# Kernel optimization log

Hardware: AMD Instinct MI355X
Metric: run time of the kernel (lower is better)

The kernel has to match this reference:

```python
import jax, jax.numpy as jnp
import numpy as np

N = 500000   # nodes (total bases across sequences)
E = 2 * N    # edges, degree-2 sequence graph
F = 128      # filters
BN_EPS = 1e-3  # Keras BatchNormalization default epsilon


def setup_inputs() -> dict:
    key = jax.random.key(0)
    ks = jax.random.split(key, 10)
    x = jax.random.normal(ks[0], (N, F), jnp.float32)
    # segment ids: sorted, each node appears twice (tf.math.segment_sum requires sorted ids)
    seg = jnp.repeat(jnp.arange(N, dtype=jnp.int32), 2)
    pairs_prev = jnp.stack([seg, jax.random.randint(ks[1], (E,), 0, N, jnp.int32)], axis=1)
    pairs_next = jnp.stack([seg, jax.random.randint(ks[2], (E,), 0, N, jnp.int32)], axis=1)
    s = 0.05  # 'random_normal' initializer stddev
    wNext = jax.random.normal(ks[3], (F, F), jnp.float32) * s
    wPrev = jax.random.normal(ks[4], (F, F), jnp.float32) * s
    b = jnp.zeros((1, F), jnp.float32)
    # GRUCell(F): kernel [F,3F], recurrent_kernel [F,3F], bias [2,3F] (reset_after=True)
    gru_kernel = jax.random.normal(ks[5], (F, 3 * F), jnp.float32) * s
    gru_recurrent_kernel = jax.random.normal(ks[6], (F, 3 * F), jnp.float32) * s
    gru_bias = jnp.zeros((2, 3 * F), jnp.float32)
    bn_gamma = jnp.ones((F,), jnp.float32)
    bn_beta = jnp.zeros((F,), jnp.float32)
    bn_mean = jax.random.normal(ks[7], (F,), jnp.float32) * 0.05
    bn_var = jnp.ones((F,), jnp.float32) + jax.random.uniform(ks[8], (F,), jnp.float32) * 0.1
    return {"x": x, "pairs_prev": pairs_prev, "pairs_next": pairs_next,
            "wNext": wNext, "wPrev": wPrev, "b": b,
            "gru_kernel": gru_kernel, "gru_recurrent_kernel": gru_recurrent_kernel,
            "gru_bias": gru_bias, "bn_gamma": bn_gamma, "bn_beta": bn_beta,
            "bn_mean": bn_mean, "bn_var": bn_var}


def reference(x, pairs_prev, pairs_next, wNext, wPrev, b,
              gru_kernel, gru_recurrent_kernel, gru_bias,
              bn_gamma, bn_beta, bn_mean, bn_var):
    n = x.shape[0]
    # gather neighbor features + segment_sum aggregation
    prev_sumx = jax.ops.segment_sum(x[pairs_prev[:, 1]], pairs_prev[:, 0], num_segments=n)
    next_sumx = jax.ops.segment_sum(x[pairs_next[:, 1]], pairs_next[:, 0], num_segments=n)
    # aggre = next@Wn + prev@Wp + b ; non-padded, multiply=False -> + x
    aggre = next_sumx @ wNext + prev_sumx @ wPrev + b + x
    # activation then BatchNorm (inference mode, training=False)
    a = jax.nn.relu(aggre)
    a = bn_gamma * (a - bn_mean) * jax.lax.rsqrt(bn_var + BN_EPS) + bn_beta
    # GRUCell(F) update with state h = x (Keras reset_after=True)
    mx = a @ gru_kernel + gru_bias[0]        # [N, 3F]
    mh = x @ gru_recurrent_kernel + gru_bias[1]
    xz, xr, xh = jnp.split(mx, 3, axis=-1)
    rz, rr, rh = jnp.split(mh, 3, axis=-1)
    z = jax.nn.sigmoid(xz + rz)
    r = jax.nn.sigmoid(xr + rr)
    hh = jnp.tanh(xh + r * rh)
    return z * x + (1.0 - z) * hh
```

## Files before the change

### kernel.cpp

```cpp
#include <hip/hip_runtime.h>
#include <hip/hip_bf16.h>
#include <stdint.h>

#define FDIM 128
#define AS1 __attribute__((address_space(1)))
#define AS3 __attribute__((address_space(3)))

typedef short bf16x8 __attribute__((ext_vector_type(8)));
typedef float f32x4 __attribute__((ext_vector_type(4)));
typedef float f32x2 __attribute__((ext_vector_type(2)));

__device__ __forceinline__ unsigned short f2bf(float f) {
    union { float f; unsigned int u; } v; v.f = f;
    unsigned int r = v.u + 0x7FFFu + ((v.u >> 16) & 1u);
    return (unsigned short)(r >> 16);
}
__device__ __forceinline__ unsigned int pack2bf(float a, float b) {
    return (unsigned int)f2bf(a) | ((unsigned int)f2bf(b) << 16);
}
__device__ __forceinline__ float bf2f(unsigned short u) {
    union { unsigned int u; float f; } v; v.u = (unsigned int)u << 16; return v.f;
}
__device__ __forceinline__ uint2 sum4fp8(unsigned int w0, unsigned int w1) {
    f32x2 a0 = __builtin_amdgcn_cvt_pk_f32_fp8((int)w0, false);
    f32x2 a1 = __builtin_amdgcn_cvt_pk_f32_fp8((int)w0, true);
    f32x2 b0 = __builtin_amdgcn_cvt_pk_f32_fp8((int)w1, false);
    f32x2 b1 = __builtin_amdgcn_cvt_pk_f32_fp8((int)w1, true);
    float s0 = a0.x + b0.x, s1 = a0.y + b0.y;
    float s2 = a1.x + b1.x, s3 = a1.y + b1.y;
    uint2 r;
    asm("v_cvt_pk_bf16_f32 %0, %1, %2" : "=v"(r.x) : "v"(s0), "v"(s1));
    asm("v_cvt_pk_bf16_f32 %0, %1, %2" : "=v"(r.y) : "v"(s2), "v"(s3));
    return r;
}

__global__ void prep_kernel(const float* __restrict__ wNext, const float* __restrict__ wPrev,
                            const float* __restrict__ gk, const float* __restrict__ gr,
                            const float* __restrict__ gb, const float* __restrict__ gamma,
                            const float* __restrict__ beta, const float* __restrict__ mean,
                            const float* __restrict__ var,
                            unsigned short* __restrict__ bt1, unsigned short* __restrict__ bt2,
                            float* __restrict__ bias2, float* __restrict__ bnscale,
                            float* __restrict__ bnshift)
{
    int t = blockIdx.x * blockDim.x + threadIdx.x;
    if (t < 32768) {
        int n = t >> 8, k = t & 255;
        float v = (k < 128) ? wNext[k * 128 + n] : wPrev[(k - 128) * 128 + n];
        unsigned int byte = (unsigned)n * 512u + (((unsigned)(k * 2)) ^ (((unsigned)(n & 15)) << 4));
        *(unsigned short*)((unsigned char*)bt1 + byte) = f2bf(v);
    } else if (t < 32768 + 131072) {
        int e = t - 32768;
        int n = e >> 8, k = e & 255;
        float v;
        if (n < 256)      v = (k < 128) ? gk[k * 384 + n] : gr[(k - 128) * 384 + n];
        else if (n < 384) v = (k < 128) ? gk[k * 384 + n] : 0.f;
        else              v = (k < 128) ? 0.f : gr[(k - 128) * 384 + (n - 128)];
        int g = n >> 7, fl = n & 127;
        int nn = ((fl >> 4) << 6) + (g << 4) + (fl & 15);
        unsigned int byte = (unsigned)nn * 512u + (((unsigned)(k * 2)) ^ (((unsigned)(nn & 15)) << 4));
        *(unsigned short*)((unsigned char*)bt2 + byte) = f2bf(v);
    } else if (t < 32768 + 131072 + 512) {
        int n = t - (32768 + 131072);
        float v;
        if (n < 256)      v = gb[n] + gb[384 + n];
        else if (n < 384) v = gb[n];
        else              v = gb[384 + (n - 128)];
        bias2[n] = v;
    } else if (t < 32768 + 131072 + 512 + 128) {
        int f = t - (32768 + 131072 + 512);
        float s = gamma[f] * rsqrtf(var[f] + 1e-3f);
        bnscale[f] = s;
        bnshift[f] = beta[f] - mean[f] * s;
    }
}

__global__ __launch_bounds__(256) void x_convert(const float* __restrict__ x,
                                                 unsigned short* __restrict__ xbf,
                                                 unsigned char* __restrict__ xq, int Nn)
{
    const int total = Nn * 16;
    const float4* x4 = (const float4*)x;
    for (int t = blockIdx.x * 256 + threadIdx.x; t < total; t += gridDim.x * 256) {
        int m = t >> 4, l = t & 15;
        float4 v0 = x4[m * 32 + l * 2];
        float4 v1 = x4[m * 32 + l * 2 + 1];
        uint4 pk;
        pk.x = pack2bf(v0.x, v0.y); pk.y = pack2bf(v0.z, v0.w);
        pk.z = pack2bf(v1.x, v1.y); pk.w = pack2bf(v1.z, v1.w);
        unsigned int byte = (unsigned)m * 256u + (((unsigned)(l * 16)) ^ (((unsigned)(m & 15)) << 4));
        *(uint4*)((unsigned char*)xbf + byte) = pk;
        int q0 = __builtin_amdgcn_cvt_pk_fp8_f32(v0.x, v0.y, 0, false);
        q0 = __builtin_amdgcn_cvt_pk_fp8_f32(v0.z, v0.w, q0, true);
        int q1 = __builtin_amdgcn_cvt_pk_fp8_f32(v1.x, v1.y, 0, false);
        q1 = __builtin_amdgcn_cvt_pk_fp8_f32(v1.z, v1.w, q1, true);
        uint2 qq; qq.x = (unsigned)q0; qq.y = (unsigned)q1;
        *(uint2*)(xq + (size_t)m * 128u + (unsigned)(l * 8)) = qq;
    }
}

__attribute__((amdgpu_waves_per_eu(4, 8)))
__global__ __launch_bounds__(512) void k_gather_g1(
    const unsigned short* __restrict__ xbf, const unsigned char* __restrict__ xq,
    const int* __restrict__ pprev, const int* __restrict__ pnext,
    const unsigned short* __restrict__ bt1,
    const float* __restrict__ bvec, const float* __restrict__ bnscale,
    const float* __restrict__ bnshift,
    unsigned short* __restrict__ a_out, int Nn)
{
    __shared__ __align__(16) unsigned char lds[49152];
    const int tid = threadIdx.x, wid = tid >> 6, lane = tid & 63;
    const int col0 = lane & 15, kq = lane >> 4;
    const unsigned int rs = (unsigned)col0 << 4;

    const unsigned char* bt1b = (const unsigned char*)bt1;
    bf16x8 b1[8];
#pragma unroll
    for (int kk = 0; kk < 8; kk++)
        b1[kk] = *(const bf16x8*)(bt1b + (unsigned)(wid * 16 + col0) * 512u +
                                  (((unsigned)(kk * 64 + kq * 16)) ^ rs));
#pragma unroll
    for (int kk = 0; kk < 8; kk++) asm volatile("" : "+v"(b1[kk]));

    const int f = wid * 16 + col0;
    const float bb = bvec[f], sc = bnscale[f], sh = bnshift[f];

    const int rg = tid >> 3, s8 = tid & 7, dirp = s8 >> 2, pg = s8 & 3;
    const int* pid = dirp ? pprev : pnext;
    const unsigned char* xb = (const unsigned char*)xbf;

    const int G = (int)gridDim.x;
    const int tiles = (Nn + 63) >> 6;

    uint4 q0a, q0b, q1a, q1b;
    int4 idxA = {0, 0, 0, 0}, idxB;
    { int gn = blockIdx.x * 64 + rg; if (gn < Nn) idxA = *(const int4*)(pid + (size_t)4 * gn); }

    for (int t = blockIdx.x; t < tiles; t += G) {
        const int base = t * 64;
        {
            size_t xg = (size_t)base * 256u + (unsigned)(wid * 2048) + (unsigned)(lane * 16);
            __builtin_amdgcn_global_load_lds((const AS1 unsigned int*)(xb + xg),
                (AS3 unsigned int*)(lds + 32768u + (unsigned)(wid * 2048)), 16, 0, 0);
            __builtin_amdgcn_global_load_lds((const AS1 unsigned int*)(xb + xg + 1024),
                (AS3 unsigned int*)(lds + 32768u + (unsigned)(wid * 2048) + 1024u), 16, 0, 0);
        }
        {
            const unsigned char* r0 = xq + (size_t)idxA.y * 128u + (unsigned)(pg * 32);
            const unsigned char* r1 = xq + (size_t)idxA.w * 128u + (unsigned)(pg * 32);
            q0a = *(const uint4*)(r0);
            q0b = *(const uint4*)(r0 + 16);
            q1a = *(const uint4*)(r1);
            q1b = *(const uint4*)(r1 + 16);
        }
        __builtin_amdgcn_sched_barrier(0);
        idxB = (int4){0, 0, 0, 0};
        {
            int gn = (t + G) * 64 + rg;
            if (t + G < tiles && gn < Nn) idxB = *(const int4*)(pid + (size_t)4 * gn);
        }
        __builtin_amdgcn_sched_barrier(0);
        asm volatile("s_waitcnt vmcnt(1)" ::: "memory");
        __builtin_amdgcn_sched_barrier(0);
        {
            unsigned char* Sd = lds + (unsigned)(rg * 512 + dirp * 256);
            unsigned swd = ((unsigned)(rg & 15)) << 4;
            uint2 e0, e1;
            uint4 d;
            e0 = sum4fp8(q0a.x, q1a.x); e1 = sum4fp8(q0a.y, q1a.y);
            d.x = e0.x; d.y = e0.y; d.z = e1.x; d.w = e1.y;
            *(uint4*)(Sd + (((unsigned)(pg * 64 + 0)) ^ swd)) = d;
            e0 = sum4fp8(q0a.z, q1a.z); e1 = sum4fp8(q0a.w, q1a.w);
            d.x = e0.x; d.y = e0.y; d.z = e1.x; d.w = e1.y;
            *(uint4*)(Sd + (((unsigned)(pg * 64 + 16)) ^ swd)) = d;
            e0 = sum4fp8(q0b.x, q1b.x); e1 = sum4fp8(q0b.y, q1b.y);
            d.x = e0.x; d.y = e0.y; d.z = e1.x; d.w = e1.y;
            *(uint4*)(Sd + (((unsigned)(pg * 64 + 32)) ^ swd)) = d;
            e0 = sum4fp8(q0b.z, q1b.z); e1 = sum4fp8(q0b.w, q1b.w);
            d.x = e0.x; d.y = e0.y; d.z = e1.x; d.w = e1.y;
            *(uint4*)(Sd + (((unsigned)(pg * 64 + 48)) ^ swd)) = d;
        }
        asm volatile("s_waitcnt lgkmcnt(0)" ::: "memory");
        __builtin_amdgcn_sched_barrier(0);
        __builtin_amdgcn_s_barrier();

        f32x4 acc1[4];
#pragma unroll
        for (int m = 0; m < 4; m++) acc1[m] = (f32x4){bb, bb, bb, bb};
#pragma unroll
        for (int kk = 0; kk < 8; kk++) {
            unsigned ko = ((unsigned)(kk * 64 + kq * 16)) ^ rs;
            bf16x8 a0 = *(const bf16x8*)(lds + (unsigned)(0 * 16 + col0) * 512u + ko);
            bf16x8 a1 = *(const bf16x8*)(lds + (unsigned)(1 * 16 + col0) * 512u + ko);
            bf16x8 a2 = *(const bf16x8*)(lds + (unsigned)(2 * 16 + col0) * 512u + ko);
            bf16x8 a3 = *(const bf16x8*)(lds + (unsigned)(3 * 16 + col0) * 512u + ko);
            acc1[0] = __builtin_amdgcn_mfma_f32_16x16x32_bf16(a0, b1[kk], acc1[0], 0, 0, 0);
            acc1[1] = __builtin_amdgcn_mfma_f32_16x16x32_bf16(a1, b1[kk], acc1[1], 0, 0, 0);
            acc1[2] = __builtin_amdgcn_mfma_f32_16x16x32_bf16(a2, b1[kk], acc1[2], 0, 0, 0);
            acc1[3] = __builtin_amdgcn_mfma_f32_16x16x32_bf16(a3, b1[kk], acc1[3], 0, 0, 0);
        }
        {
            const unsigned char* X = lds + 32768u;
#pragma unroll
            for (int m = 0; m < 4; m++) {
#pragma unroll
                for (int i = 0; i < 4; i++) {
                    int r = m * 16 + kq * 4 + i;
                    int grow = base + r;
                    if (grow < Nn) {
                        unsigned sw = ((unsigned)(r & 15)) << 4;
                        unsigned co = ((unsigned)(f * 2)) ^ sw;
                        float xv = bf2f(*(const unsigned short*)(X + (unsigned)r * 256u + co));
                        float v = acc1[m][i] + xv;
                        v = fmaxf(v, 0.f) * sc + sh;
                        __builtin_nontemporal_store(
                            f2bf(v),
                            (unsigned short*)((unsigned char*)a_out + (size_t)grow * 256u + co));
                    }
                }
            }
        }
        __builtin_amdgcn_s_barrier();
        idxA = idxB;
    }
}

__attribute__((amdgpu_waves_per_eu(2, 2)))
__global__ __launch_bounds__(512) void k_g2_gru(
    const unsigned short* __restrict__ a_in, const unsigned short* __restrict__ xbf,
    const unsigned short* __restrict__ bt2p, const float* __restrict__ bias2,
    float* __restrict__ out, int Nn)
{
    __shared__ __align__(16) unsigned char lds[65536];
    const int tid = threadIdx.x, wid = tid >> 6, lane = tid & 63;
    const int col0 = lane & 15, kq = lane >> 4;
    const unsigned int rs = (unsigned)col0 << 4;

    const unsigned char* bt2b = (const unsigned char*)bt2p;
    bf16x8 b2z[8], b2r[8], b2xh[4], b2rh[4];
#pragma unroll
    for (int kk = 0; kk < 8; kk++) {
        b2z[kk] = *(const bf16x8*)(bt2b + (unsigned)(wid * 64 + 0 + col0) * 512u + (((unsigned)(kk * 64 + kq * 16)) ^ rs));
        b2r[kk] = *(const bf16x8*)(bt2b + (unsigned)(wid * 64 + 16 + col0) * 512u + (((unsigned)(kk * 64 + kq * 16)) ^ rs));
    }
#pragma unroll
    for (int kk = 0; kk < 4; kk++) {
        b2xh[kk] = *(const bf16x8*)(bt2b + (unsigned)(wid * 64 + 32 + col0) * 512u + (((unsigned)(kk * 64 + kq * 16)) ^ rs));
        b2rh[kk] = *(const bf16x8*)(bt2b + (unsigned)(wid * 64 + 48 + col0) * 512u + (((unsigned)((kk + 4) * 64 + kq * 16)) ^ rs));
    }
#pragma unroll
    for (int kk = 0; kk < 8; kk++) {
        asm volatile("" : "+v"(b2z[kk]));
        asm volatile("" : "+v"(b2r[kk]));
    }
#pragma unroll
    for (int kk = 0; kk < 4; kk++) {
        asm volatile("" : "+v"(b2xh[kk]));
        asm volatile("" : "+v"(b2rh[kk]));
    }

    const int f = wid * 16 + col0;
    const float cz = bias2[f], cr = bias2[128 + f], cxh = bias2[256 + f], crh = bias2[384 + f];

    const unsigned char* aB = (const unsigned char*)a_in;
    const unsigned char* xB = (const unsigned char*)xbf;
    const int G = (int)gridDim.x;
    const int tiles = (Nn + 63) >> 6;

#define STAGE2(tt, pp) do {                                                                  \
    size_t g_ = (size_t)(tt) * 16384u + (unsigned)(wid * 2048) + (unsigned)(lane * 16);      \
    unsigned o_ = (unsigned)(pp) * 32768u + (unsigned)(wid * 2048);                          \
    __builtin_amdgcn_global_load_lds((const AS1 unsigned int*)(aB + g_),                     \
                                     (AS3 unsigned int*)(lds + o_), 16, 0, 0);               \
    __builtin_amdgcn_global_load_lds((const AS1 unsigned int*)(aB + g_ + 1024),              \
                                     (AS3 unsigned int*)(lds + o_ + 1024), 16, 0, 0);        \
    __builtin_amdgcn_global_load_lds((const AS1 unsigned int*)(xB + g_),                     \
                                     (AS3 unsigned int*)(lds + o_ + 16384u), 16, 0, 0);      \
    __builtin_amdgcn_global_load_lds((const AS1 unsigned int*)(xB + g_ + 1024),              \
                                     (AS3 unsigned int*)(lds + o_ + 16384u + 1024), 16, 0, 0);\
} while (0)

    STAGE2(blockIdx.x, 0);
    asm volatile("s_waitcnt vmcnt(0)" ::: "memory");
    __builtin_amdgcn_sched_barrier(0);
    __builtin_amdgcn_s_barrier();

    int p = 0;
    for (int t = blockIdx.x; t < tiles; t += G) {
        const int base = t * 64;
        {
            int tn = t + G;
            int tc = (tn < tiles) ? tn : t;
            STAGE2(tc, p ^ 1);
        }
        const unsigned char* A_ = lds + (unsigned)p * 32768u;
        const unsigned char* X_ = lds + (unsigned)p * 32768u + 16384u;

#pragma unroll
        for (int half = 0; half < 2; half++) {
            f32x4 az[2], ar[2], axh[2], arh[2];
#pragma unroll
            for (int mm = 0; mm < 2; mm++) {
                az[mm]  = (f32x4){cz, cz, cz, cz};
                ar[mm]  = (f32x4){cr, cr, cr, cr};
                axh[mm] = (f32x4){cxh, cxh, cxh, cxh};
                arh[mm] = (f32x4){crh, crh, crh, crh};
            }
#pragma unroll
            for (int kk = 0; kk < 8; kk++) {
                bf16x8 a2f[2];
#pragma unroll
                for (int mm = 0; mm < 2; mm++) {
                    int m = half * 2 + mm;
                    if (kk < 4)
                        a2f[mm] = *(const bf16x8*)(A_ + (unsigned)(m * 16 + col0) * 256u +
                                                   (((unsigned)(kk * 64 + kq * 16)) ^ rs));
                    else
                        a2f[mm] = *(const bf16x8*)(X_ + (unsigned)(m * 16 + col0) * 256u +
                                                   (((unsigned)((kk - 4) * 64 + kq * 16)) ^ rs));
                }
#pragma unroll
                for (int mm = 0; mm < 2; mm++) {
                    az[mm] = __builtin_amdgcn_mfma_f32_16x16x32_bf16(a2f[mm], b2z[kk], az[mm], 0, 0, 0);
                    ar[mm] = __builtin_amdgcn_mfma_f32_16x16x32_bf16(a2f[mm], b2r[kk], ar[mm], 0, 0, 0);
                    if (kk < 4)
                        axh[mm] = __builtin_amdgcn_mfma_f32_16x16x32_bf16(a2f[mm], b2xh[kk], axh[mm], 0, 0, 0);
                    else
                        arh[mm] = __builtin_amdgcn_mfma_f32_16x16x32_bf16(a2f[mm], b2rh[kk - 4], arh[mm], 0, 0, 0);
                }
            }
#pragma unroll
            for (int mm = 0; mm < 2; mm++) {
                int m = half * 2 + mm;
#pragma unroll
                for (int i = 0; i < 4; i++) {
                    int r = m * 16 + kq * 4 + i;
                    int grow = base + r;
                    if (grow < Nn) {
                        float z  = __builtin_amdgcn_rcpf(1.f + __expf(-az[mm][i]));
                        float rr = __builtin_amdgcn_rcpf(1.f + __expf(-ar[mm][i]));
                        float u  = axh[mm][i] + rr * arh[mm][i];
                        float th = 1.f - 2.f * __builtin_amdgcn_rcpf(__expf(2.f * u) + 1.f);
                        unsigned sw = ((unsigned)(r & 15)) << 4;
                        float xv = bf2f(*(const unsigned short*)(X_ + (unsigned)r * 256u +
                                                                 (((unsigned)(f * 2)) ^ sw)));
                        __builtin_nontemporal_store(th + z * (xv - th),
                                                    out + (size_t)grow * FDIM + f);
                    }
                }
            }
        }
        asm volatile("s_waitcnt vmcnt(16) lgkmcnt(0)" ::: "memory");
        __builtin_amdgcn_sched_barrier(0);
        __builtin_amdgcn_s_barrier();
        p ^= 1;
    }
#undef STAGE2
}

extern "C" void kernel_launch(void* const* d_in, const int* in_sizes, int n_in,
                              void* d_out, int out_size, void* d_ws, size_t ws_size,
                              hipStream_t stream)
{
    const float* x      = (const float*)d_in[0];
    const int*   pprev  = (const int*)d_in[1];
    const int*   pnext  = (const int*)d_in[2];
    const float* wNext  = (const float*)d_in[3];
    const float* wPrev  = (const float*)d_in[4];
    const float* b      = (const float*)d_in[5];
    const float* gk     = (const float*)d_in[6];
    const float* gr     = (const float*)d_in[7];
    const float* gb     = (const float*)d_in[8];
    const float* gamma  = (const float*)d_in[9];
    const float* beta   = (const float*)d_in[10];
    const float* mean   = (const float*)d_in[11];
    const float* var    = (const float*)d_in[12];
    float* out = (float*)d_out;
    const int Nn = in_sizes[0] / FDIM;

    unsigned char* ws = (unsigned char*)d_ws;
    unsigned short* xbf  = (unsigned short*)(ws + 0);
    unsigned short* a_ws = (unsigned short*)(ws + (size_t)Nn * 256u);
    unsigned char*  xq   = (unsigned char*)(ws + (size_t)Nn * 512u);
    size_t off_bt = (size_t)Nn * 640u;
    unsigned short* bt1   = (unsigned short*)(ws + off_bt);
    unsigned short* bt2   = (unsigned short*)(ws + off_bt + 65536);
    float* bias2          = (float*)(ws + off_bt + 327680);
    float* bnscale        = (float*)(ws + off_bt + 327680 + 2048);
    float* bnshift        = (float*)(ws + off_bt + 327680 + 2048 + 512);

    prep_kernel<<<643, 256, 0, stream>>>(wNext, wPrev, gk, gr, gb, gamma, beta, mean, var,
                                         bt1, bt2, bias2, bnscale, bnshift);
    x_convert<<<2048, 256, 0, stream>>>(x, xbf, xq, Nn);
    k_gather_g1<<<768, 512, 0, stream>>>(xbf, xq, pprev, pnext, bt1, b, bnscale, bnshift, a_ws, Nn);
    k_g2_gru<<<256, 512, 0, stream>>>(a_ws, xbf, bt2, bias2, out, Nn);
}
```

Measured before the change: 330.1 us.

## Software-pipeline neighbor gather and x staging one tile ahead in gather kernel

Restructures the gather+GEMM1 loop so the fp8 neighbor gathers and index loads for the next tile (and indices two tiles ahead) are issued before the current tile's MFMA work. x tiles are double-buffered in LDS, which grows from 48KB to 64KB, so the async x copy for tile t+G overlaps the current tile's compute and epilogue. The goal is to hide random-gather latency behind compute. The larger LDS footprint reduces occupancy, and the grid shrinks from 768 to 512 blocks to match. Hand-tuned vmcnt waits must match the exact load counts, which is fragile.

```diff
diff --git a/kernel.cpp b/kernel.cpp
--- a/kernel.cpp
+++ b/kernel.cpp
@@ -108,7 +108,7 @@
     const float* __restrict__ bnshift,
     unsigned short* __restrict__ a_out, int Nn)
 {
-    __shared__ __align__(16) unsigned char lds[49152];
+    __shared__ __align__(16) unsigned char lds[65536];
     const int tid = threadIdx.x, wid = tid >> 6, lane = tid & 63;
     const int col0 = lane & 15, kq = lane >> 4;
     const unsigned int rs = (unsigned)col0 << 4;
@@ -133,56 +133,77 @@
     const int tiles = (Nn + 63) >> 6;
 
     uint4 q0a, q0b, q1a, q1b;
-    int4 idxA = {0, 0, 0, 0}, idxB;
-    { int gn = blockIdx.x * 64 + rg; if (gn < Nn) idxA = *(const int4*)(pid + (size_t)4 * gn); }
-
+    int4 idxN, idxN2;
+
+#define STAGE_X(tt, slot) do {                                                              \
+    size_t xg_ = (size_t)(tt) * 16384u + (unsigned)(wid * 2048) + (unsigned)(lane * 16);    \
+    unsigned xo_ = 32768u + (unsigned)(slot) * 16384u + (unsigned)(wid * 2048);             \
+    __builtin_amdgcn_global_load_lds((const AS1 unsigned int*)(xb + xg_),                   \
+                                     (AS3 unsigned int*)(lds + xo_), 16, 0, 0);             \
+    __builtin_amdgcn_global_load_lds((const AS1 unsigned int*)(xb + xg_ + 1024),            \
+                                     (AS3 unsigned int*)(lds + xo_ + 1024), 16, 0, 0);      \
+} while (0)
+
+#define GATHER_ISSUE(ix) do {                                                               \
+    const unsigned char* r0_ = xq + (size_t)(ix).y * 128u + (unsigned)(pg * 32);            \
+    const unsigned char* r1_ = xq + (size_t)(ix).w * 128u + (unsigned)(pg * 32);            \
+    q0a = *(const uint4*)(r0_);                                                             \
+    q0b = *(const uint4*)(r0_ + 16);                                                        \
+    q1a = *(const uint4*)(r1_);                                                             \
+    q1b = *(const uint4*)(r1_ + 16);                                                        \
+} while (0)
+
+#define IDX_LOAD(dst, tc) do {                                                              \
+    (dst) = (int4){0, 0, 0, 0};                                                             \
+    int gn_ = (tc) * 64 + rg;                                                               \
+    if ((tc) < tiles && gn_ < Nn) (dst) = *(const int4*)(pid + (size_t)4 * gn_);            \
+} while (0)
+
+#define SUM_WRITE() do {                                                                    \
+    unsigned char* Sd_ = lds + (unsigned)(rg * 512 + dirp * 256);                           \
+    unsigned swd_ = ((unsigned)(rg & 15)) << 4;                                             \
+    uint2 e0_, e1_; uint4 d_;                                                               \
+    e0_ = sum4fp8(q0a.x, q1a.x); e1_ = sum4fp8(q0a.y, q1a.y);                               \
+    d_.x = e0_.x; d_.y = e0_.y; d_.z = e1_.x; d_.w = e1_.y;                                 \
+    *(uint4*)(Sd_ + (((unsigned)(pg * 64 + 0)) ^ swd_)) = d_;                               \
+    e0_ = sum4fp8(q0a.z, q1a.z); e1_ = sum4fp8(q0a.w, q1a.w);                               \
+    d_.x = e0_.x; d_.y = e0_.y; d_.z = e1_.x; d_.w = e1_.y;                                 \
+    *(uint4*)(Sd_ + (((unsigned)(pg * 64 + 16)) ^ swd_)) = d_;                              \
+    e0_ = sum4fp8(q0b.x, q1b.x); e1_ = sum4fp8(q0b.y, q1b.y);                               \
+    d_.x = e0_.x; d_.y = e0_.y; d_.z = e1_.x; d_.w = e1_.y;                                 \
+    *(uint4*)(Sd_ + (((unsigned)(pg * 64 + 32)) ^ swd_)) = d_;                              \
+    e0_ = sum4fp8(q0b.z, q1b.z); e1_ = sum4fp8(q0b.w, q1b.w);                               \
+    d_.x = e0_.x; d_.y = e0_.y; d_.z = e1_.x; d_.w = e1_.y;                                 \
+    *(uint4*)(Sd_ + (((unsigned)(pg * 64 + 48)) ^ swd_)) = d_;                              \
+} while (0)
+
+    {
+        int4 idx0 = (int4){0, 0, 0, 0};
+        int gn = blockIdx.x * 64 + rg;
+        if (gn < Nn) idx0 = *(const int4*)(pid + (size_t)4 * gn);
+        GATHER_ISSUE(idx0);
+        IDX_LOAD(idxN, (int)blockIdx.x + G);
+        STAGE_X(blockIdx.x, 0);
+        __builtin_amdgcn_sched_barrier(0);
+        asm volatile("s_waitcnt vmcnt(0)" ::: "memory");
+        __builtin_amdgcn_sched_barrier(0);
+        SUM_WRITE();
+        asm volatile("s_waitcnt lgkmcnt(0)" ::: "memory");
+        __builtin_amdgcn_sched_barrier(0);
+        __builtin_amdgcn_s_barrier();
+    }
+
+    int xs = 0;
     for (int t = blockIdx.x; t < tiles; t += G) {
         const int base = t * 64;
+        GATHER_ISSUE(idxN);
+        IDX_LOAD(idxN2, t + 2 * G);
+        __builtin_amdgcn_sched_barrier(0);
         {
-            size_t xg = (size_t)base * 256u + (unsigned)(wid * 2048) + (unsigned)(lane * 16);
-            __builtin_amdgcn_global_load_lds((const AS1 unsigned int*)(xb + xg),
-                (AS3 unsigned int*)(lds + 32768u + (unsigned)(wid * 2048)), 16, 0, 0);
-            __builtin_amdgcn_global_load_lds((const AS1 unsigned int*)(xb + xg + 1024),
-                (AS3 unsigned int*)(lds + 32768u + (unsigned)(wid * 2048) + 1024u), 16, 0, 0);
+            int tc = t + G; if (tc >= tiles) tc = t;
+            STAGE_X(tc, xs ^ 1);
         }
-        {
-            const unsigned char* r0 = xq + (size_t)idxA.y * 128u + (unsigned)(pg * 32);
-            const unsigned char* r1 = xq + (size_t)idxA.w * 128u + (unsigned)(pg * 32);
-            q0a = *(const uint4*)(r0);
-            q0b = *(const uint4*)(r0 + 16);
-            q1a = *(const uint4*)(r1);
-            q1b = *(const uint4*)(r1 + 16);
-        }
-        __builtin_amdgcn_sched_barrier(0);
-        idxB = (int4){0, 0, 0, 0};
-        {
-            int gn = (t + G) * 64 + rg;
-            if (t + G < tiles && gn < Nn) idxB = *(const int4*)(pid + (size_t)4 * gn);
-        }
-        __builtin_amdgcn_sched_barrier(0);
-        asm volatile("s_waitcnt vmcnt(1)" ::: "memory");
-        __builtin_amdgcn_sched_barrier(0);
-        {
-            unsigned char* Sd = lds + (unsigned)(rg * 512 + dirp * 256);
-            unsigned swd = ((unsigned)(rg & 15)) << 4;
-            uint2 e0, e1;
-            uint4 d;
-            e0 = sum4fp8(q0a.x, q1a.x); e1 = sum4fp8(q0a.y, q1a.y);
-            d.x = e0.x; d.y = e0.y; d.z = e1.x; d.w = e1.y;
-            *(uint4*)(Sd + (((unsigned)(pg * 64 + 0)) ^ swd)) = d;
-            e0 = sum4fp8(q0a.z, q1a.z); e1 = sum4fp8(q0a.w, q1a.w);
-            d.x = e0.x; d.y = e0.y; d.z = e1.x; d.w = e1.y;
-            *(uint4*)(Sd + (((unsigned)(pg * 64 + 16)) ^ swd)) = d;
-            e0 = sum4fp8(q0b.x, q1b.x); e1 = sum4fp8(q0b.y, q1b.y);
-            d.x = e0.x; d.y = e0.y; d.z = e1.x; d.w = e1.y;
-            *(uint4*)(Sd + (((unsigned)(pg * 64 + 32)) ^ swd)) = d;
-            e0 = sum4fp8(q0b.z, q1b.z); e1 = sum4fp8(q0b.w, q1b.w);
-            d.x = e0.x; d.y = e0.y; d.z = e1.x; d.w = e1.y;
-            *(uint4*)(Sd + (((unsigned)(pg * 64 + 48)) ^ swd)) = d;
-        }
-        asm volatile("s_waitcnt lgkmcnt(0)" ::: "memory");
-        __builtin_amdgcn_sched_barrier(0);
-        __builtin_amdgcn_s_barrier();
+        __builtin_amdgcn_sched_barrier(0);
 
         f32x4 acc1[4];
 #pragma unroll
@@ -200,7 +221,7 @@
             acc1[3] = __builtin_amdgcn_mfma_f32_16x16x32_bf16(a3, b1[kk], acc1[3], 0, 0, 0);
         }
         {
-            const unsigned char* X = lds + 32768u;
+            const unsigned char* X = lds + 32768u + (unsigned)xs * 16384u;
 #pragma unroll
             for (int m = 0; m < 4; m++) {
 #pragma unroll
@@ -220,9 +241,23 @@
                 }
             }
         }
+        __builtin_amdgcn_sched_barrier(0);
+        asm volatile("s_waitcnt vmcnt(18) lgkmcnt(0)" ::: "memory");
+        __builtin_amdgcn_sched_barrier(0);
         __builtin_amdgcn_s_barrier();
-        idxA = idxB;
-    }
+        SUM_WRITE();
+        asm volatile("s_waitcnt lgkmcnt(0)" ::: "memory");
+        __builtin_amdgcn_sched_barrier(0);
+        asm volatile("s_waitcnt vmcnt(16)" ::: "memory");
+        __builtin_amdgcn_sched_barrier(0);
+        __builtin_amdgcn_s_barrier();
+        xs ^= 1;
+        idxN = idxN2;
+    }
+#undef STAGE_X
+#undef GATHER_ISSUE
+#undef IDX_LOAD
+#undef SUM_WRITE
 }
 
 __attribute__((amdgpu_waves_per_eu(2, 2)))
@@ -392,6 +427,6 @@
     prep_kernel<<<643, 256, 0, stream>>>(wNext, wPrev, gk, gr, gb, gamma, beta, mean, var,
                                          bt1, bt2, bias2, bnscale, bnshift);
     x_convert<<<2048, 256, 0, stream>>>(x, xbf, xq, Nn);
-    k_gather_g1<<<768, 512, 0, stream>>>(xbf, xq, pprev, pnext, bt1, b, bnscale, bnshift, a_ws, Nn);
+    k_gather_g1<<<512, 512, 0, stream>>>(xbf, xq, pprev, pnext, bt1, b, bnscale, bnshift, a_ws, Nn);
     k_g2_gru<<<256, 512, 0, stream>>>(a_ws, xbf, bt2, bias2, out, Nn);
 }
```

Measured after the change: 407.4 us. 1.23x slower.

## Warp-specialize gather kernel into producer and MFMA consumer waves with double-buffered LDS

Applied to the files above, without the earlier changes.

The fused gather+GEMM kernel is split so that waves 0-3 only gather the fp8 neighbour rows, sum them into LDS and copy the x tile, while waves 4-7 only run the bf16 MFMA and the ReLU/BN epilogue. Each consumer wave now covers 32 output columns. The tile shrinks from 64 to 32 rows and the LDS staging is double-buffered, so the gather for tile k+1 can overlap the matrix multiply for tile k with one barrier per tile. The grid drops from 768 to 512 blocks. The risks are that only half the waves issue gather loads, and the smaller tile raises barrier and per-tile overhead.

```diff
diff --git a/kernel.cpp b/kernel.cpp
--- a/kernel.cpp
+++ b/kernel.cpp
@@ -110,118 +110,147 @@
 {
     __shared__ __align__(16) unsigned char lds[49152];
     const int tid = threadIdx.x, wid = tid >> 6, lane = tid & 63;
-    const int col0 = lane & 15, kq = lane >> 4;
-    const unsigned int rs = (unsigned)col0 << 4;
-
-    const unsigned char* bt1b = (const unsigned char*)bt1;
-    bf16x8 b1[8];
-#pragma unroll
-    for (int kk = 0; kk < 8; kk++)
-        b1[kk] = *(const bf16x8*)(bt1b + (unsigned)(wid * 16 + col0) * 512u +
-                                  (((unsigned)(kk * 64 + kq * 16)) ^ rs));
-#pragma unroll
-    for (int kk = 0; kk < 8; kk++) asm volatile("" : "+v"(b1[kk]));
-
-    const int f = wid * 16 + col0;
-    const float bb = bvec[f], sc = bnscale[f], sh = bnshift[f];
-
-    const int rg = tid >> 3, s8 = tid & 7, dirp = s8 >> 2, pg = s8 & 3;
-    const int* pid = dirp ? pprev : pnext;
-    const unsigned char* xb = (const unsigned char*)xbf;
-
     const int G = (int)gridDim.x;
-    const int tiles = (Nn + 63) >> 6;
-
-    uint4 q0a, q0b, q1a, q1b;
-    int4 idxA = {0, 0, 0, 0}, idxB;
-    { int gn = blockIdx.x * 64 + rg; if (gn < Nn) idxA = *(const int4*)(pid + (size_t)4 * gn); }
-
-    for (int t = blockIdx.x; t < tiles; t += G) {
-        const int base = t * 64;
-        {
-            size_t xg = (size_t)base * 256u + (unsigned)(wid * 2048) + (unsigned)(lane * 16);
-            __builtin_amdgcn_global_load_lds((const AS1 unsigned int*)(xb + xg),
-                (AS3 unsigned int*)(lds + 32768u + (unsigned)(wid * 2048)), 16, 0, 0);
-            __builtin_amdgcn_global_load_lds((const AS1 unsigned int*)(xb + xg + 1024),
-                (AS3 unsigned int*)(lds + 32768u + (unsigned)(wid * 2048) + 1024u), 16, 0, 0);
-        }
-        {
-            const unsigned char* r0 = xq + (size_t)idxA.y * 128u + (unsigned)(pg * 32);
-            const unsigned char* r1 = xq + (size_t)idxA.w * 128u + (unsigned)(pg * 32);
-            q0a = *(const uint4*)(r0);
-            q0b = *(const uint4*)(r0 + 16);
-            q1a = *(const uint4*)(r1);
-            q1b = *(const uint4*)(r1 + 16);
-        }
-        __builtin_amdgcn_sched_barrier(0);
-        idxB = (int4){0, 0, 0, 0};
-        {
-            int gn = (t + G) * 64 + rg;
-            if (t + G < tiles && gn < Nn) idxB = *(const int4*)(pid + (size_t)4 * gn);
-        }
-        __builtin_amdgcn_sched_barrier(0);
-        asm volatile("s_waitcnt vmcnt(1)" ::: "memory");
-        __builtin_amdgcn_sched_barrier(0);
-        {
-            unsigned char* Sd = lds + (unsigned)(rg * 512 + dirp * 256);
-            unsigned swd = ((unsigned)(rg & 15)) << 4;
-            uint2 e0, e1;
-            uint4 d;
-            e0 = sum4fp8(q0a.x, q1a.x); e1 = sum4fp8(q0a.y, q1a.y);
-            d.x = e0.x; d.y = e0.y; d.z = e1.x; d.w = e1.y;
-            *(uint4*)(Sd + (((unsigned)(pg * 64 + 0)) ^ swd)) = d;
-            e0 = sum4fp8(q0a.z, q1a.z); e1 = sum4fp8(q0a.w, q1a.w);
-            d.x = e0.x; d.y = e0.y; d.z = e1.x; d.w = e1.y;
-            *(uint4*)(Sd + (((unsigned)(pg * 64 + 16)) ^ swd)) = d;
-            e0 = sum4fp8(q0b.x, q1b.x); e1 = sum4fp8(q0b.y, q1b.y);
-            d.x = e0.x; d.y = e0.y; d.z = e1.x; d.w = e1.y;
-            *(uint4*)(Sd + (((unsigned)(pg * 64 + 32)) ^ swd)) = d;
-            e0 = sum4fp8(q0b.z, q1b.z); e1 = sum4fp8(q0b.w, q1b.w);
-            d.x = e0.x; d.y = e0.y; d.z = e1.x; d.w = e1.y;
-            *(uint4*)(Sd + (((unsigned)(pg * 64 + 48)) ^ swd)) = d;
-        }
-        asm volatile("s_waitcnt lgkmcnt(0)" ::: "memory");
-        __builtin_amdgcn_sched_barrier(0);
+    const int tiles = (Nn + 31) >> 5;
+    const int bid = (int)blockIdx.x;
+    const int ntb = (tiles - bid + G - 1) / G;
+
+    if (wid < 4) {
+        const int ptid = tid;
+        const int rg = ptid >> 3, s8 = ptid & 7, dirp = s8 >> 2, pg = s8 & 3;
+        const int* pid = dirp ? pprev : pnext;
+        const unsigned char* xb = (const unsigned char*)xbf;
+
+        uint4 q0a, q0b, q1a, q1b;
+        int4 idxA = {0, 0, 0, 0}, idxB;
+        { int gn = bid * 32 + rg; if (gn < Nn) idxA = *(const int4*)(pid + (size_t)4 * gn); }
+
+        for (int k = 0; k < ntb; k++) {
+            const int t = bid + k * G;
+            const int dstp = k & 1;
+            {
+                size_t xg = (size_t)t * 8192u + (unsigned)(ptid * 16);
+                unsigned xo = 32768u + (unsigned)dstp * 8192u + (unsigned)(ptid * 16);
+                __builtin_amdgcn_global_load_lds((const AS1 unsigned int*)(xb + xg),
+                                                 (AS3 unsigned int*)(lds + xo), 16, 0, 0);
+                __builtin_amdgcn_global_load_lds((const AS1 unsigned int*)(xb + xg + 4096),
+                                                 (AS3 unsigned int*)(lds + xo + 4096), 16, 0, 0);
+            }
+            {
+                const unsigned char* r0 = xq + (size_t)idxA.y * 128u + (unsigned)(pg * 32);
+                const unsigned char* r1 = xq + (size_t)idxA.w * 128u + (unsigned)(pg * 32);
+                q0a = *(const uint4*)(r0);
+                q0b = *(const uint4*)(r0 + 16);
+                q1a = *(const uint4*)(r1);
+                q1b = *(const uint4*)(r1 + 16);
+            }
+            __builtin_amdgcn_sched_barrier(0);
+            idxB = (int4){0, 0, 0, 0};
+            {
+                int tn = t + G;
+                int gn = tn * 32 + rg;
+                if (tn < tiles && gn < Nn) idxB = *(const int4*)(pid + (size_t)4 * gn);
+            }
+            __builtin_amdgcn_sched_barrier(0);
+            asm volatile("s_waitcnt vmcnt(1)" ::: "memory");
+            __builtin_amdgcn_sched_barrier(0);
+            {
+                unsigned char* Sd = lds + (unsigned)dstp * 16384u + (unsigned)(rg * 512 + dirp * 256);
+                unsigned swd = ((unsigned)(rg & 15)) << 4;
+                uint2 e0, e1;
+                uint4 d;
+                e0 = sum4fp8(q0a.x, q1a.x); e1 = sum4fp8(q0a.y, q1a.y);
+                d.x = e0.x; d.y = e0.y; d.z = e1.x; d.w = e1.y;
+                *(uint4*)(Sd + (((unsigned)(pg * 64 + 0)) ^ swd)) = d;
+                e0 = sum4fp8(q0a.z, q1a.z); e1 = sum4fp8(q0a.w, q1a.w);
+                d.x = e0.x; d.y = e0.y; d.z = e1.x; d.w = e1.y;
+                *(uint4*)(Sd + (((unsigned)(pg * 64 + 16)) ^ swd)) = d;
+                e0 = sum4fp8(q0b.x, q1b.x); e1 = sum4fp8(q0b.y, q1b.y);
+                d.x = e0.x; d.y = e0.y; d.z = e1.x; d.w = e1.y;
+                *(uint4*)(Sd + (((unsigned)(pg * 64 + 32)) ^ swd)) = d;
+                e0 = sum4fp8(q0b.z, q1b.z); e1 = sum4fp8(q0b.w, q1b.w);
+                d.x = e0.x; d.y = e0.y; d.z = e1.x; d.w = e1.y;
+                *(uint4*)(Sd + (((unsigned)(pg * 64 + 48)) ^ swd)) = d;
+            }
+            asm volatile("s_waitcnt lgkmcnt(0)" ::: "memory");
+            __builtin_amdgcn_sched_barrier(0);
+            idxA = idxB;
+            __builtin_amdgcn_s_barrier();
+        }
         __builtin_amdgcn_s_barrier();
-
-        f32x4 acc1[4];
-#pragma unroll
-        for (int m = 0; m < 4; m++) acc1[m] = (f32x4){bb, bb, bb, bb};
+    } else {
+        const int cw = wid - 4;
+        const int col0 = lane & 15, kq = lane >> 4;
+        const unsigned int rs = (unsigned)col0 << 4;
+        const unsigned char* bt1b = (const unsigned char*)bt1;
+
+        bf16x8 b1a[8], b1b[8];
 #pragma unroll
         for (int kk = 0; kk < 8; kk++) {
-            unsigned ko = ((unsigned)(kk * 64 + kq * 16)) ^ rs;
-            bf16x8 a0 = *(const bf16x8*)(lds + (unsigned)(0 * 16 + col0) * 512u + ko);
-            bf16x8 a1 = *(const bf16x8*)(lds + (unsigned)(1 * 16 + col0) * 512u + ko);
-            bf16x8 a2 = *(const bf16x8*)(lds + (unsigned)(2 * 16 + col0) * 512u + ko);
-            bf16x8 a3 = *(const bf16x8*)(lds + (unsigned)(3 * 16 + col0) * 512u + ko);
-            acc1[0] = __builtin_amdgcn_mfma_f32_16x16x32_bf16(a0, b1[kk], acc1[0], 0, 0, 0);
-            acc1[1] = __builtin_amdgcn_mfma_f32_16x16x32_bf16(a1, b1[kk], acc1[1], 0, 0, 0);
-            acc1[2] = __builtin_amdgcn_mfma_f32_16x16x32_bf16(a2, b1[kk], acc1[2], 0, 0, 0);
-            acc1[3] = __builtin_amdgcn_mfma_f32_16x16x32_bf16(a3, b1[kk], acc1[3], 0, 0, 0);
-        }
-        {
-            const unsigned char* X = lds + 32768u;
-#pragma unroll
-            for (int m = 0; m < 4; m++) {
+            b1a[kk] = *(const bf16x8*)(bt1b + (unsigned)(cw * 32 + col0) * 512u +
+                                       (((unsigned)(kk * 64 + kq * 16)) ^ rs));
+            b1b[kk] = *(const bf16x8*)(bt1b + (unsigned)(cw * 32 + 16 + col0) * 512u +
+                                       (((unsigned)(kk * 64 + kq * 16)) ^ rs));
+        }
+#pragma unroll
+        for (int kk = 0; kk < 8; kk++) {
+            asm volatile("" : "+v"(b1a[kk]));
+            asm volatile("" : "+v"(b1b[kk]));
+        }
+
+        const int f0 = cw * 32 + col0, f1 = f0 + 16;
+        const float bb0 = bvec[f0], sc0 = bnscale[f0], sh0 = bnshift[f0];
+        const float bb1 = bvec[f1], sc1 = bnscale[f1], sh1 = bnshift[f1];
+
+        for (int k = 0; k < ntb; k++) {
+            __builtin_amdgcn_s_barrier();
+            const int t = bid + k * G;
+            const int p = k & 1;
+            const unsigned char* S = lds + (unsigned)p * 16384u;
+            const unsigned char* X = lds + 32768u + (unsigned)p * 8192u;
+
+            f32x4 acc00 = (f32x4){bb0, bb0, bb0, bb0};
+            f32x4 acc01 = (f32x4){bb1, bb1, bb1, bb1};
+            f32x4 acc10 = (f32x4){bb0, bb0, bb0, bb0};
+            f32x4 acc11 = (f32x4){bb1, bb1, bb1, bb1};
+#pragma unroll
+            for (int kk = 0; kk < 8; kk++) {
+                unsigned ko = ((unsigned)(kk * 64 + kq * 16)) ^ rs;
+                bf16x8 a0 = *(const bf16x8*)(S + (unsigned)(col0) * 512u + ko);
+                bf16x8 a1 = *(const bf16x8*)(S + (unsigned)(16 + col0) * 512u + ko);
+                acc00 = __builtin_amdgcn_mfma_f32_16x16x32_bf16(a0, b1a[kk], acc00, 0, 0, 0);
+                acc10 = __builtin_amdgcn_mfma_f32_16x16x32_bf16(a1, b1a[kk], acc10, 0, 0, 0);
+                acc01 = __builtin_amdgcn_mfma_f32_16x16x32_bf16(a0, b1b[kk], acc01, 0, 0, 0);
+                acc11 = __builtin_amdgcn_mfma_f32_16x16x32_bf16(a1, b1b[kk], acc11, 0, 0, 0);
+            }
+            const int base = t * 32;
+#pragma unroll
+            for (int m = 0; m < 2; m++) {
 #pragma unroll
                 for (int i = 0; i < 4; i++) {
                     int r = m * 16 + kq * 4 + i;
                     int grow = base + r;
                     if (grow < Nn) {
                         unsigned sw = ((unsigned)(r & 15)) << 4;
-                        unsigned co = ((unsigned)(f * 2)) ^ sw;
-                        float xv = bf2f(*(const unsigned short*)(X + (unsigned)r * 256u + co));
-                        float v = acc1[m][i] + xv;
-                        v = fmaxf(v, 0.f) * sc + sh;
+                        unsigned co0 = ((unsigned)(f0 * 2)) ^ sw;
+                        unsigned co1 = ((unsigned)(f1 * 2)) ^ sw;
+                        float a0v = (m == 0) ? acc00[i] : acc10[i];
+                        float a1v = (m == 0) ? acc01[i] : acc11[i];
+                        float xv0 = bf2f(*(const unsigned short*)(X + (unsigned)r * 256u + co0));
+                        float xv1 = bf2f(*(const unsigned short*)(X + (unsigned)r * 256u + co1));
+                        float v0 = fmaxf(a0v + xv0, 0.f) * sc0 + sh0;
+                        float v1 = fmaxf(a1v + xv1, 0.f) * sc1 + sh1;
                         __builtin_nontemporal_store(
-                            f2bf(v),
-                            (unsigned short*)((unsigned char*)a_out + (size_t)grow * 256u + co));
+                            f2bf(v0),
+                            (unsigned short*)((unsigned char*)a_out + (size_t)grow * 256u + co0));
+                        __builtin_nontemporal_store(
+                            f2bf(v1),
+                            (unsigned short*)((unsigned char*)a_out + (size_t)grow * 256u + co1));
                     }
                 }
             }
         }
         __builtin_amdgcn_s_barrier();
-        idxA = idxB;
     }
 }
 
@@ -392,6 +421,6 @@
     prep_kernel<<<643, 256, 0, stream>>>(wNext, wPrev, gk, gr, gb, gamma, beta, mean, var,
                                          bt1, bt2, bias2, bnscale, bnshift);
     x_convert<<<2048, 256, 0, stream>>>(x, xbf, xq, Nn);
-    k_gather_g1<<<768, 512, 0, stream>>>(xbf, xq, pprev, pnext, bt1, b, bnscale, bnshift, a_ws, Nn);
+    k_gather_g1<<<512, 512, 0, stream>>>(xbf, xq, pprev, pnext, bt1, b, bnscale, bnshift, a_ws, Nn);
     k_g2_gru<<<256, 512, 0, stream>>>(a_ws, xbf, bt2, bias2, out, Nn);
 }
```

New measurement: 380.2 us. +15.2%, slower.
